# Performance work log

Hardware: AMD Instinct MI355X
Metric: run time of the kernel (lower is better)

## Reference

```python
import jax, jax.numpy as jnp
import numpy as np

G = 7          # grid_size
A = 2          # anchors_per_cell
C = 3          # num_classes
L_COORD, L_OBJ, L_NOOBJ, L_CLS = 5.0, 1.0, 0.5, 2.0


def setup_inputs() -> dict:
    key = jax.random.key(0)
    k0, k1, k2, k3, k4 = jax.random.split(key, 5)
    B, M = 32768, 20
    predictions = jax.random.normal(k0, (B, G, G, A, 5 + C), dtype=jnp.float32)
    xy1 = jax.random.uniform(k1, (B, M, 2), dtype=jnp.float32) * 0.8
    wh = jax.random.uniform(k2, (B, M, 2), dtype=jnp.float32) * 0.19 + 0.01
    target_boxes = jnp.concatenate([xy1, xy1 + wh], axis=-1)  # valid x1<x2, y1<y2
    target_labels = jax.random.randint(k3, (B, M), 0, C, dtype=jnp.int32)
    num_objs = jax.random.randint(k4, (B,), 0, M + 1, dtype=jnp.int32)
    anchors = jnp.array([[0.971, 1.7338], [3.4579, 5.1653]], dtype=jnp.float32)
    class_weights = jnp.array([1.0, 4.9, 4.8], dtype=jnp.float32)
    return dict(predictions=predictions, target_boxes=target_boxes,
                target_labels=target_labels, num_objs=num_objs,
                anchors=anchors, class_weights=class_weights)


def assign_targets(target_boxes, target_labels, num_objs, anchors, B):
    """Vectorized scatter-based replacement of the nested python assignment loop."""
    M = target_boxes.shape[1]
    x1, y1, x2, y2 = [target_boxes[..., i] for i in range(4)]  # (B,M)
    cx, cy = (x1 + x2) * 0.5, (y1 + y2) * 0.5
    w, h = x2 - x1, y2 - y1
    valid = (w > 0) & (h > 0) & (jnp.arange(M)[None, :] < num_objs[:, None])
    gi = jnp.clip(jnp.floor(cy * G).astype(jnp.int32), 0, G - 1)
    gj = jnp.clip(jnp.floor(cx * G).astype(jnp.int32), 0, G - 1)
    wg, hg = w * G, h * G
    # anchor matching IoU (width/height only), (B,M,A)
    inter = jnp.minimum(wg[..., None], anchors[:, 0]) * jnp.minimum(hg[..., None], anchors[:, 1])
    union = (wg * hg)[..., None] + anchors[:, 0] * anchors[:, 1] - inter
    best_a = jnp.argmax(inter / (union + 1e-6), axis=-1).astype(jnp.int32)  # first max = torch loop tie-break
    aw = anchors[best_a, 0]
    ah = anchors[best_a, 1]
    tx = cx * G - gj.astype(jnp.float32)
    ty = cy * G - gi.astype(jnp.float32)
    tw = jnp.log(jnp.clip(wg, 0.01, None) / (aw + 1e-6))
    th = jnp.log(jnp.clip(hg, 0.01, None) / (ah + 1e-6))
    tvals = jnp.stack([tx, ty, tw, th], axis=-1)  # (B,M,4)
    N = B * G * G * A
    bidx = jnp.arange(B, dtype=jnp.int32)[:, None]
    flat = ((bidx * G + gi) * G + gj) * A + best_a  # (B,M)
    flat = jnp.where(valid, flat, N)                # invalid -> dropped by scatter
    idx = flat.ravel()
    obj_mask = jnp.zeros((N,), jnp.float32).at[idx].set(1.0, mode='drop')
    target_bbox = jnp.zeros((N, 4), jnp.float32).at[idx].set(tvals.reshape(-1, 4), mode='drop')
    target_cls = jnp.zeros((N,), jnp.int32).at[idx].set(target_labels.ravel(), mode='drop')
    shape = (B, G, G, A)
    return obj_mask.reshape(shape), target_bbox.reshape(shape + (4,)), target_cls.reshape(shape)


def reference(predictions, target_boxes, target_labels, num_objs, anchors, class_weights):
    B = predictions.shape[0]
    pred_obj = predictions[..., 0]
    pred_bbox = predictions[..., 1:5]
    pred_cls = predictions[..., 5:]
    m, target_bbox, target_cls = assign_targets(target_boxes, target_labels, num_objs, anchors, B)
    sp = jax.nn.softplus
    # BCE-with-logits: target is 1 on obj cells, 0 on noobj cells
    loss_obj = jnp.sum(m * sp(-pred_obj))
    loss_noobj = jnp.sum((1.0 - m) * sp(pred_obj))
    # smooth L1 (beta=1), summed over obj cells
    d = pred_bbox - target_bbox
    ad = jnp.abs(d)
    sl1 = jnp.where(ad < 1.0, 0.5 * d * d, ad - 0.5)
    loss_bbox = jnp.sum(m[..., None] * sl1)
    # weighted cross entropy on obj cells
    logZ = jax.nn.logsumexpimport if False else jax.scipy.special.logsumexp(pred_cls, axis=-1)
    logit_t = jnp.take_along_axis(pred_cls, target_cls[..., None], axis=-1)[..., 0]
    loss_cls = jnp.sum(m * class_weights[target_cls] * (logZ - logit_t))
    num_pos = jnp.maximum(jnp.sum(m), 1.0)
    total = (L_COORD * loss_bbox + L_OBJ * loss_obj + L_NOOBJ * loss_noobj + L_CLS * loss_cls) / num_pos
    return total
```

## Files before the change

### kernel.cpp

```cpp
#include <hip/hip_runtime.h>


namespace {
constexpr int kG = 7;
constexpr int kA = 2;
constexpr int kM = 20;
constexpr int kCells = kG * kG * kA;
constexpr int kCh = 8;
constexpr int kNBatch = 5;
constexpr int kBlock = 512;
constexpr int kTgtB = kNBatch * kM;
constexpr int kCellsB = kNBatch * kCells;
}

__device__ __forceinline__ float softplus_fast(float x) {
    return fmaxf(x, 0.0f) + __logf(1.0f + __expf(-fabsf(x)));
}

__global__ __launch_bounds__(kBlock) void det_loss_main(
    const float* __restrict__ preds,
    const float* __restrict__ tboxes,
    const int* __restrict__ tlabels,
    const int* __restrict__ nobjs,
    const float* __restrict__ anchors,
    const float* __restrict__ cweights,
    float* __restrict__ partial,
    int B)
{
    __shared__ float4 s_tv[kTgtB + 1];
    __shared__ float  s_cw[kTgtB + 1];
    __shared__ int    s_lab[kTgtB + 1];
    __shared__ short  s_cell[kTgtB];
    __shared__ short  s_table[kCellsB];
    __shared__ float  s_red[kBlock / 64][5];

    const int tid = threadIdx.x;
    const int b0 = blockIdx.x * kNBatch;
    const int nAct = min(kNBatch, B - b0) * kCells;

    if (tid < kCellsB) s_table[tid] = -1;
    if (tid == kBlock - 1) {
        s_tv[kTgtB] = make_float4(0.f, 0.f, 0.f, 0.f);
        s_cw[kTgtB] = 0.f;
        s_lab[kTgtB] = 0;
    }

    const float a00 = anchors[0], a01 = anchors[1];
    const float a10 = anchors[2], a11 = anchors[3];

    if (tid < kTgtB) {
        const int bl = tid / kM;
        const int m  = tid - bl * kM;
        const int b  = b0 + bl;
        short cell = -1;
        float4 tv = make_float4(0.f, 0.f, 0.f, 0.f);
        float cwv = 0.f;
        int lab = 0;
        if (b < B && m < nobjs[b]) {
            const float4 box = ((const float4*)tboxes)[(size_t)b * kM + m];
            const float x1 = box.x, y1 = box.y, x2 = box.z, y2 = box.w;
            const float cx = (x1 + x2) * 0.5f, cy = (y1 + y2) * 0.5f;
            const float w = x2 - x1, h = y2 - y1;
            if (w > 0.f && h > 0.f) {
                const int gi = min(max((int)floorf(cy * (float)kG), 0), kG - 1);
                const int gj = min(max((int)floorf(cx * (float)kG), 0), kG - 1);
                const float wg = w * (float)kG, hg = h * (float)kG;
                const float i0 = fminf(wg, a00) * fminf(hg, a01);
                const float u0 = wg * hg + a00 * a01 - i0;
                const float r0 = i0 / (u0 + 1e-6f);
                const float i1 = fminf(wg, a10) * fminf(hg, a11);
                const float u1 = wg * hg + a10 * a11 - i1;
                const float r1 = i1 / (u1 + 1e-6f);
                const int a = (r1 > r0) ? 1 : 0;
                const float aw = a ? a10 : a00;
                const float ah = a ? a11 : a01;
                tv.x = cx * (float)kG - (float)gj;
                tv.y = cy * (float)kG - (float)gi;
                tv.z = __logf(fmaxf(wg, 0.01f) / (aw + 1e-6f));
                tv.w = __logf(fmaxf(hg, 0.01f) / (ah + 1e-6f));
                cell = (short)(bl * kCells + (gi * kG + gj) * kA + a);
                lab = tlabels[(size_t)b * kM + m];
                cwv = cweights[lab];
            }
        }
        s_cell[tid] = cell;
        s_tv[tid] = tv;
        s_cw[tid] = cwv;
        s_lab[tid] = lab;
    }
    __syncthreads();

    if (tid < kTgtB) {
        const short c = s_cell[tid];
        if (c >= 0) {
            const int bl = tid / kM;
            const int m  = tid - bl * kM;
            bool win = true;
            for (int m2 = m + 1; m2 < kM; ++m2) {
                if (s_cell[bl * kM + m2] == c) { win = false; break; }
            }
            if (win) s_table[c] = (short)tid;
        }
    }
    __syncthreads();

    float accO = 0.f, accN = 0.f, accB = 0.f, accC = 0.f, npf = 0.f;
    if (tid < nAct) {
        const float4* __restrict__ pc =
            (const float4*)preds + ((size_t)b0 * kCells + tid) * 2;
        const float4 p0 = pc[0];
        const float4 p1 = pc[1];
        const int j = s_table[tid];
        const bool pos = (j >= 0);
        const int jj = pos ? j : kTgtB;
        const float m = pos ? 1.f : 0.f;
        const float4 tv = s_tv[jj];
        const float cwv = s_cw[jj];
        const int lab = s_lab[jj];

        const float po = p0.x;
        const float spo = softplus_fast(po);
        accN = spo - m * spo;
        accO = m * (spo - po);

        float d, ad, sb;
        d = p0.y - tv.x; ad = fabsf(d); sb  = (ad < 1.f) ? 0.5f * d * d : ad - 0.5f;
        d = p0.z - tv.y; ad = fabsf(d); sb += (ad < 1.f) ? 0.5f * d * d : ad - 0.5f;
        d = p0.w - tv.z; ad = fabsf(d); sb += (ad < 1.f) ? 0.5f * d * d : ad - 0.5f;
        d = p1.x - tv.w; ad = fabsf(d); sb += (ad < 1.f) ? 0.5f * d * d : ad - 0.5f;
        accB = m * sb;

        const float c0 = p1.y, c1 = p1.z, c2 = p1.w;
        const float mx = fmaxf(c0, fmaxf(c1, c2));
        const float lse = mx + __logf(__expf(c0 - mx) + __expf(c1 - mx) + __expf(c2 - mx));
        const float logit = (lab == 0) ? c0 : ((lab == 1) ? c1 : c2);
        accC = m * cwv * (lse - logit);
        npf = m;
    }

    float vals[5] = {accO, accN, accB, accC, npf};
    #pragma unroll
    for (int k = 0; k < 5; ++k) {
        float v = vals[k];
        #pragma unroll
        for (int off = 32; off > 0; off >>= 1) v += __shfl_down(v, off, 64);
        vals[k] = v;
    }
    const int wave = tid >> 6;
    const int lane = tid & 63;
    if (lane == 0) {
        #pragma unroll
        for (int k = 0; k < 5; ++k) s_red[wave][k] = vals[k];
    }
    __syncthreads();
    if (tid == 0) {
        float t[5];
        #pragma unroll
        for (int k = 0; k < 5; ++k) {
            float s = 0.f;
            #pragma unroll
            for (int w = 0; w < kBlock / 64; ++w) s += s_red[w][k];
            t[k] = s;
        }
        float4* p4o = (float4*)(partial + (size_t)blockIdx.x * 8);
        p4o[0] = make_float4(t[0], t[1], t[2], t[3]);
        p4o[1] = make_float4(t[4], 0.f, 0.f, 0.f);
    }
}

__global__ __launch_bounds__(1024) void det_loss_reduce(
    const float* __restrict__ partial, int nblocks, float* __restrict__ out)
{
    __shared__ float s_red[16][5];
    const int tid = threadIdx.x;
    const float4* __restrict__ p4 = (const float4*)partial;
    float v[5] = {0.f, 0.f, 0.f, 0.f, 0.f};
    for (int e = tid; e < nblocks; e += 1024) {
        const float4 a = p4[2 * e];
        const float4 b = p4[2 * e + 1];
        v[0] += a.x; v[1] += a.y; v[2] += a.z; v[3] += a.w; v[4] += b.x;
    }
    #pragma unroll
    for (int k = 0; k < 5; ++k) {
        float x = v[k];
        #pragma unroll
        for (int off = 32; off > 0; off >>= 1) x += __shfl_down(x, off, 64);
        v[k] = x;
    }
    const int wave = tid >> 6;
    const int lane = tid & 63;
    if (lane == 0) {
        #pragma unroll
        for (int k = 0; k < 5; ++k) s_red[wave][k] = v[k];
    }
    __syncthreads();
    if (tid == 0) {
        float t[5];
        #pragma unroll
        for (int k = 0; k < 5; ++k) {
            float s = 0.f;
            #pragma unroll
            for (int w = 0; w < 16; ++w) s += s_red[w][k];
            t[k] = s;
        }
        const float npv = fmaxf(t[4], 1.0f);
        out[0] = (5.0f * t[2] + 1.0f * t[0] + 0.5f * t[1] + 2.0f * t[3]) / npv;
    }
}

extern "C" void kernel_launch(void* const* d_in, const int* in_sizes, int n_in,
                              void* d_out, int out_size, void* d_ws, size_t ws_size,
                              hipStream_t stream) {
    const float* preds    = (const float*)d_in[0];
    const float* tboxes   = (const float*)d_in[1];
    const int*   tlabels  = (const int*)d_in[2];
    const int*   nobjs    = (const int*)d_in[3];
    const float* anchors  = (const float*)d_in[4];
    const float* cweights = (const float*)d_in[5];
    float* out = (float*)d_out;
    float* partial = (float*)d_ws;

    const int B = in_sizes[0] / (kCells * kCh);
    const int blocks = (B + kNBatch - 1) / kNBatch;

    det_loss_main<<<blocks, kBlock, 0, stream>>>(
        preds, tboxes, tlabels, nobjs, anchors, cweights, partial, B);
    det_loss_reduce<<<1, 1024, 0, stream>>>(partial, blocks, out);
}
```

Before: 188.4 us.

## Split fused loss kernel into separate target-assignment and cell-streaming kernels

The single fused kernel is replaced by two kernels. The first assigns targets for 32 images per block and writes a per-cell winner table and per-target records (box offsets, class weight, label) to workspace. The second streams all prediction cells with small 256-thread blocks and gathers the records only for positive cells. The aim is to take the serialized assignment phase and its block-wide barriers out of the bandwidth-bound prediction read so that memory latency is hidden better. The cost is extra global writes and reads of the table and records, plus one more kernel launch.

New measurement: 188.0 us. About the same (-0.2%).

```diff
diff --git a/kernel.cpp b/kernel.cpp
--- a/kernel.cpp
+++ b/kernel.cpp
@@ -7,116 +7,121 @@
 constexpr int kM = 20;
 constexpr int kCells = kG * kG * kA;
 constexpr int kCh = 8;
-constexpr int kNBatch = 5;
-constexpr int kBlock = 512;
-constexpr int kTgtB = kNBatch * kM;
-constexpr int kCellsB = kNBatch * kCells;
+constexpr int kABat = 32;
+constexpr int kABlock = kABat * kM;
+constexpr int kBBlock = 256;
 }
 
 __device__ __forceinline__ float softplus_fast(float x) {
     return fmaxf(x, 0.0f) + __logf(1.0f + __expf(-fabsf(x)));
 }
 
-__global__ __launch_bounds__(kBlock) void det_loss_main(
-    const float* __restrict__ preds,
+__global__ __launch_bounds__(kABlock) void det_assign(
     const float* __restrict__ tboxes,
     const int* __restrict__ tlabels,
     const int* __restrict__ nobjs,
     const float* __restrict__ anchors,
     const float* __restrict__ cweights,
-    float* __restrict__ partial,
+    short* __restrict__ table,
+    float4* __restrict__ rec,
     int B)
 {
-    __shared__ float4 s_tv[kTgtB + 1];
-    __shared__ float  s_cw[kTgtB + 1];
-    __shared__ int    s_lab[kTgtB + 1];
-    __shared__ short  s_cell[kTgtB];
-    __shared__ short  s_table[kCellsB];
-    __shared__ float  s_red[kBlock / 64][5];
+    __shared__ short s_cell[kABlock];
 
     const int tid = threadIdx.x;
-    const int b0 = blockIdx.x * kNBatch;
-    const int nAct = min(kNBatch, B - b0) * kCells;
-
-    if (tid < kCellsB) s_table[tid] = -1;
-    if (tid == kBlock - 1) {
-        s_tv[kTgtB] = make_float4(0.f, 0.f, 0.f, 0.f);
-        s_cw[kTgtB] = 0.f;
-        s_lab[kTgtB] = 0;
+    const int b0 = blockIdx.x * kABat;
+
+    {
+        int* tp = (int*)(table + (size_t)b0 * kCells);
+        const int nInt = kABat * kCells / 2;
+        for (int i = tid; i < nInt; i += kABlock) tp[i] = -1;
     }
 
     const float a00 = anchors[0], a01 = anchors[1];
     const float a10 = anchors[2], a11 = anchors[3];
 
-    if (tid < kTgtB) {
-        const int bl = tid / kM;
-        const int m  = tid - bl * kM;
-        const int b  = b0 + bl;
-        short cell = -1;
-        float4 tv = make_float4(0.f, 0.f, 0.f, 0.f);
-        float cwv = 0.f;
-        int lab = 0;
-        if (b < B && m < nobjs[b]) {
-            const float4 box = ((const float4*)tboxes)[(size_t)b * kM + m];
-            const float x1 = box.x, y1 = box.y, x2 = box.z, y2 = box.w;
-            const float cx = (x1 + x2) * 0.5f, cy = (y1 + y2) * 0.5f;
-            const float w = x2 - x1, h = y2 - y1;
-            if (w > 0.f && h > 0.f) {
-                const int gi = min(max((int)floorf(cy * (float)kG), 0), kG - 1);
-                const int gj = min(max((int)floorf(cx * (float)kG), 0), kG - 1);
-                const float wg = w * (float)kG, hg = h * (float)kG;
-                const float i0 = fminf(wg, a00) * fminf(hg, a01);
-                const float u0 = wg * hg + a00 * a01 - i0;
-                const float r0 = i0 / (u0 + 1e-6f);
-                const float i1 = fminf(wg, a10) * fminf(hg, a11);
-                const float u1 = wg * hg + a10 * a11 - i1;
-                const float r1 = i1 / (u1 + 1e-6f);
-                const int a = (r1 > r0) ? 1 : 0;
-                const float aw = a ? a10 : a00;
-                const float ah = a ? a11 : a01;
-                tv.x = cx * (float)kG - (float)gj;
-                tv.y = cy * (float)kG - (float)gi;
-                tv.z = __logf(fmaxf(wg, 0.01f) / (aw + 1e-6f));
-                tv.w = __logf(fmaxf(hg, 0.01f) / (ah + 1e-6f));
-                cell = (short)(bl * kCells + (gi * kG + gj) * kA + a);
-                lab = tlabels[(size_t)b * kM + m];
-                cwv = cweights[lab];
-            }
-        }
-        s_cell[tid] = cell;
-        s_tv[tid] = tv;
-        s_cw[tid] = cwv;
-        s_lab[tid] = lab;
+    const int bl = tid / kM;
+    const int m  = tid - bl * kM;
+    const int b  = b0 + bl;
+
+    short cell = -1;
+    float4 tv = make_float4(0.f, 0.f, 0.f, 0.f);
+    float cwv = 0.f;
+    float labf = 0.f;
+    if (b < B && m < nobjs[b]) {
+        const float4 box = ((const float4*)tboxes)[(size_t)b * kM + m];
+        const float x1 = box.x, y1 = box.y, x2 = box.z, y2 = box.w;
+        const float cx = (x1 + x2) * 0.5f, cy = (y1 + y2) * 0.5f;
+        const float w = x2 - x1, h = y2 - y1;
+        if (w > 0.f && h > 0.f) {
+            const int gi = min(max((int)floorf(cy * (float)kG), 0), kG - 1);
+            const int gj = min(max((int)floorf(cx * (float)kG), 0), kG - 1);
+            const float wg = w * (float)kG, hg = h * (float)kG;
+            const float i0 = fminf(wg, a00) * fminf(hg, a01);
+            const float u0 = wg * hg + a00 * a01 - i0;
+            const float r0 = i0 / (u0 + 1e-6f);
+            const float i1 = fminf(wg, a10) * fminf(hg, a11);
+            const float u1 = wg * hg + a10 * a11 - i1;
+            const float r1 = i1 / (u1 + 1e-6f);
+            const int a = (r1 > r0) ? 1 : 0;
+            const float aw = a ? a10 : a00;
+            const float ah = a ? a11 : a01;
+            tv.x = cx * (float)kG - (float)gj;
+            tv.y = cy * (float)kG - (float)gi;
+            tv.z = __logf(fmaxf(wg, 0.01f) / (aw + 1e-6f));
+            tv.w = __logf(fmaxf(hg, 0.01f) / (ah + 1e-6f));
+            cell = (short)((gi * kG + gj) * kA + a);
+            const int lab = tlabels[(size_t)b * kM + m];
+            cwv = cweights[lab];
+            labf = (float)lab;
+        }
+    }
+    s_cell[tid] = cell;
+    if (b < B) {
+        rec[((size_t)b * kM + m) * 2]     = tv;
+        rec[((size_t)b * kM + m) * 2 + 1] = make_float4(cwv, labf, 0.f, 0.f);
     }
     __syncthreads();
 
-    if (tid < kTgtB) {
-        const short c = s_cell[tid];
-        if (c >= 0) {
-            const int bl = tid / kM;
-            const int m  = tid - bl * kM;
-            bool win = true;
-            for (int m2 = m + 1; m2 < kM; ++m2) {
-                if (s_cell[bl * kM + m2] == c) { win = false; break; }
-            }
-            if (win) s_table[c] = (short)tid;
-        }
-    }
-    __syncthreads();
+    if (cell >= 0) {
+        bool win = true;
+        const int base = bl * kM;
+        for (int m2 = m + 1; m2 < kM; ++m2) {
+            if (s_cell[base + m2] == cell) { win = false; break; }
+        }
+        if (win) table[(size_t)b * kCells + cell] = (short)m;
+    }
+}
+
+__global__ __launch_bounds__(kBBlock) void det_stream(
+    const float* __restrict__ preds,
+    const short* __restrict__ table,
+    const float4* __restrict__ rec,
+    float* __restrict__ partial,
+    int ncells)
+{
+    __shared__ float s_red[kBBlock / 64][5];
+
+    const int tid = threadIdx.x;
+    const int g = blockIdx.x * kBBlock + tid;
 
     float accO = 0.f, accN = 0.f, accB = 0.f, accC = 0.f, npf = 0.f;
-    if (tid < nAct) {
-        const float4* __restrict__ pc =
-            (const float4*)preds + ((size_t)b0 * kCells + tid) * 2;
+    if (g < ncells) {
+        const float4* __restrict__ pc = (const float4*)preds + (size_t)g * 2;
         const float4 p0 = pc[0];
         const float4 p1 = pc[1];
-        const int j = s_table[tid];
-        const bool pos = (j >= 0);
-        const int jj = pos ? j : kTgtB;
+        const int t = table[g];
+        const bool pos = (t >= 0);
+
+        float4 tv = make_float4(0.f, 0.f, 0.f, 0.f);
+        float4 r2 = make_float4(0.f, 0.f, 0.f, 0.f);
+        if (pos) {
+            const unsigned b = (unsigned)g / (unsigned)kCells;
+            const float4* rp = rec + ((size_t)b * kM + t) * 2;
+            tv = rp[0];
+            r2 = rp[1];
+        }
         const float m = pos ? 1.f : 0.f;
-        const float4 tv = s_tv[jj];
-        const float cwv = s_cw[jj];
-        const int lab = s_lab[jj];
 
         const float po = p0.x;
         const float spo = softplus_fast(po);
@@ -130,11 +135,12 @@
         d = p1.x - tv.w; ad = fabsf(d); sb += (ad < 1.f) ? 0.5f * d * d : ad - 0.5f;
         accB = m * sb;
 
+        const int lab = (int)r2.y;
         const float c0 = p1.y, c1 = p1.z, c2 = p1.w;
         const float mx = fmaxf(c0, fmaxf(c1, c2));
         const float lse = mx + __logf(__expf(c0 - mx) + __expf(c1 - mx) + __expf(c2 - mx));
         const float logit = (lab == 0) ? c0 : ((lab == 1) ? c1 : c2);
-        accC = m * cwv * (lse - logit);
+        accC = m * r2.x * (lse - logit);
         npf = m;
     }
 
@@ -159,7 +165,7 @@
         for (int k = 0; k < 5; ++k) {
             float s = 0.f;
             #pragma unroll
-            for (int w = 0; w < kBlock / 64; ++w) s += s_red[w][k];
+            for (int w = 0; w < kBBlock / 64; ++w) s += s_red[w][k];
             t[k] = s;
         }
         float4* p4o = (float4*)(partial + (size_t)blockIdx.x * 8);
@@ -168,7 +174,7 @@
     }
 }
 
-__global__ __launch_bounds__(1024) void det_loss_reduce(
+__global__ __launch_bounds__(1024) void det_reduce(
     const float* __restrict__ partial, int nblocks, float* __restrict__ out)
 {
     __shared__ float s_red[16][5];
@@ -218,12 +224,23 @@
     const float* anchors  = (const float*)d_in[4];
     const float* cweights = (const float*)d_in[5];
     float* out = (float*)d_out;
-    float* partial = (float*)d_ws;
 
     const int B = in_sizes[0] / (kCells * kCh);
-    const int blocks = (B + kNBatch - 1) / kNBatch;
-
-    det_loss_main<<<blocks, kBlock, 0, stream>>>(
-        preds, tboxes, tlabels, nobjs, anchors, cweights, partial, B);
-    det_loss_reduce<<<1, 1024, 0, stream>>>(partial, blocks, out);
-}
+    const int ncells = B * kCells;
+
+    char* ws = (char*)d_ws;
+    short*  table   = (short*)ws;
+    size_t  off     = (size_t)B * kCells * sizeof(short);
+    float4* rec     = (float4*)(ws + off);
+    off            += (size_t)B * kM * 2 * sizeof(float4);
+    float*  partial = (float*)(ws + off);
+
+    const int aBlocks = (B + kABat - 1) / kABat;
+    const int sBlocks = (ncells + kBBlock - 1) / kBBlock;
+
+    det_assign<<<aBlocks, kABlock, 0, stream>>>(
+        tboxes, tlabels, nobjs, anchors, cweights, table, rec, B);
+    det_stream<<<sBlocks, kBBlock, 0, stream>>>(
+        preds, table, rec, partial, ncells);
+    det_reduce<<<1, 1024, 0, stream>>>(partial, sBlocks, out);
+}
```
